# Performance work log

Hardware: AMD Instinct MI355X
Metric: run time of the kernel (lower is better)

## Reference

```python
import jax, jax.numpy as jnp
import numpy as np

# --- dims (match init_kwargs) ---
VOCAB = 16; D_MODEL = 512; NLAYERS = 4; LMAX = 1024; NCLASSES = 2
D_STATE = 128; D_CONV = 4; EXPAND = 2; HEADDIM = 64; PAD_IDX = 4
D_INNER = EXPAND * D_MODEL            # 1024
NHEADS = D_INNER // HEADDIM           # 16
CONV_DIM = D_INNER + 2 * D_STATE      # 1280 (ngroups=1)
D_IN_PROJ = 2 * D_INNER + 2 * D_STATE + NHEADS  # 2320
BATCH = 8; SEQ = 1024
EPS = 1e-5


def silu(x):
    return x * jax.nn.sigmoid(x)


def setup_inputs() -> dict:
    key = jax.random.key(0)
    ks = jax.random.split(key, 24)
    s = 0.02
    emb = jax.random.normal(ks[0], (VOCAB, D_MODEL), jnp.float32) * s
    emb = emb.at[PAD_IDX].set(0.0)  # padding_idx row is zero
    inp = {
        "tokens": jax.random.randint(ks[1], (BATCH, SEQ), 0, VOCAB),
        "attention_mask": jnp.ones((BATCH, SEQ), jnp.float32),
        "emb": emb,
        "pos_emb": jax.random.normal(ks[2], (1, LMAX, D_MODEL), jnp.float32) * s,
        "inp_w": jax.random.normal(ks[3], (D_MODEL, D_MODEL), jnp.float32) * s,
        "inp_b": jnp.zeros((D_MODEL,), jnp.float32),
        "ln_g": jnp.ones((D_MODEL,), jnp.float32),
        "ln_b": jnp.zeros((D_MODEL,), jnp.float32),
        # stacked per-layer Mamba2 params
        "in_proj_w": jax.random.normal(ks[4], (NLAYERS, D_IN_PROJ, D_MODEL), jnp.float32) * s,
        "conv_w": jax.random.normal(ks[5], (NLAYERS, CONV_DIM, D_CONV), jnp.float32) * 0.2,
        "conv_b": jnp.zeros((NLAYERS, CONV_DIM), jnp.float32),
        "dt_bias": jax.random.uniform(ks[6], (NLAYERS, NHEADS), jnp.float32, -4.0, -1.0),
        "A_log": jnp.log(jax.random.uniform(ks[7], (NLAYERS, NHEADS), jnp.float32, 1.0, 16.0)),
        "Dparam": jnp.ones((NLAYERS, NHEADS), jnp.float32),
        "norm_w": jnp.ones((NLAYERS, D_INNER), jnp.float32),
        "out_proj_w": jax.random.normal(ks[8], (NLAYERS, D_MODEL, D_INNER), jnp.float32) * s,
        "pooler_w": jax.random.normal(ks[9], (D_MODEL, D_MODEL), jnp.float32) * s,
        "pooler_b": jnp.zeros((D_MODEL,), jnp.float32),
        "cls_w1": jax.random.normal(ks[10], (D_MODEL // 2, D_MODEL), jnp.float32) * s,
        "cls_b1": jnp.zeros((D_MODEL // 2,), jnp.float32),
        "cls_w2": jax.random.normal(ks[11], (NCLASSES, D_MODEL // 2), jnp.float32) * s,
        "cls_b2": jnp.zeros((NCLASSES,), jnp.float32),
    }
    return inp


def mamba2_block(x, in_proj_w, conv_w, conv_b, dt_bias, A_log, Dp, norm_w, out_proj_w):
    """Mamba2 (ngroups=1, no proj biases, conv bias) on x:(B,L,d_model)."""
    Bsz, L, _ = x.shape
    zxbcdt = jnp.einsum("bld,ed->ble", x, in_proj_w)  # (B,L,2320)
    z = zxbcdt[..., :D_INNER]
    xBC = zxbcdt[..., D_INNER:D_INNER + CONV_DIM]
    dt = zxbcdt[..., D_INNER + CONV_DIM:]             # (B,L,H)
    # causal depthwise conv1d + silu
    xp = jnp.pad(xBC, ((0, 0), (D_CONV - 1, 0), (0, 0)))
    conv = conv_b
    for k in range(D_CONV):
        conv = conv + xp[:, k:k + L, :] * conv_w[:, k]
    xBC = silu(conv)
    xh = xBC[..., :D_INNER].reshape(Bsz, L, NHEADS, HEADDIM)
    Bc = xBC[..., D_INNER:D_INNER + D_STATE]          # (B,L,N)
    Cc = xBC[..., D_INNER + D_STATE:]                 # (B,L,N)
    dt = jax.nn.softplus(dt + dt_bias)                # (B,L,H)
    A = -jnp.exp(A_log)                               # (H,)
    dA = jnp.exp(dt * A)                              # (B,L,H)

    def step(h, inp):
        x_t, B_t, C_t, dt_t, dA_t = inp  # (B,H,P),(B,N),(B,N),(B,H),(B,H)
        h = h * dA_t[:, :, None, None] + (dt_t[:, :, None] * x_t)[..., None] * B_t[:, None, None, :]
        y = jnp.einsum("bhpn,bn->bhp", h, C_t)
        return h, y

    h0 = jnp.zeros((Bsz, NHEADS, HEADDIM, D_STATE), x.dtype)
    xs = (xh.transpose(1, 0, 2, 3), Bc.transpose(1, 0, 2), Cc.transpose(1, 0, 2),
          dt.transpose(1, 0, 2), dA.transpose(1, 0, 2))
    _, ys = jax.lax.scan(step, h0, xs)                # (L,B,H,P)
    y = ys.transpose(1, 0, 2, 3) + Dp[None, None, :, None] * xh
    y = y.reshape(Bsz, L, D_INNER)
    # gated RMSNorm: rmsnorm(y * silu(z)) * weight
    y = y * silu(z)
    y = y * jax.lax.rsqrt(jnp.mean(y * y, axis=-1, keepdims=True) + EPS) * norm_w
    return jnp.einsum("ble,de->bld", y, out_proj_w)


def reference(tokens, attention_mask, emb, pos_emb, inp_w, inp_b, ln_g, ln_b,
              in_proj_w, conv_w, conv_b, dt_bias, A_log, Dparam, norm_w, out_proj_w,
              pooler_w, pooler_b, cls_w1, cls_b1, cls_w2, cls_b2):
    L = tokens.shape[1]
    x = emb[tokens] + pos_emb[:, :L, :]
    # input_block: Linear -> LayerNorm (dropout is identity at eval)
    x = jnp.einsum("bld,ed->ble", x, inp_w) + inp_b
    mu = jnp.mean(x, -1, keepdims=True)
    var = jnp.mean((x - mu) ** 2, -1, keepdims=True)
    x = (x - mu) * jax.lax.rsqrt(var + EPS) * ln_g + ln_b
    x = x * attention_mask[..., None]
    for i in range(NLAYERS):
        res = x
        x = mamba2_block(x, in_proj_w[i], conv_w[i], conv_b[i], dt_bias[i],
                         A_log[i], Dparam[i], norm_w[i], out_proj_w[i])
        x = res + x
        x = x * attention_mask[..., None]
    pooled = (jnp.mean(x, axis=1) + jnp.max(x, axis=1)) * 0.5
    pooled = jax.nn.gelu(jnp.einsum("bd,ed->be", pooled, pooler_w) + pooler_b)
    h = jax.nn.gelu(jnp.einsum("bd,ed->be", pooled, cls_w1) + cls_b1)
    return jnp.einsum("bd,ed->be", h, cls_w2) + cls_b2
```

## Files before the change

### kernel.cpp

```cpp
#include <hip/hip_runtime.h>

#define EPS 1e-5f
typedef unsigned short u16;
typedef short s16x8 __attribute__((ext_vector_type(8)));
typedef float f32x4 __attribute__((ext_vector_type(4)));

__device__ __forceinline__ float siluf(float x) { return x / (1.0f + __expf(-x)); }
__device__ __forceinline__ float geluf(float x) {
    float u = 0.7978845608028654f * (x + 0.044715f * x * x * x);
    return 0.5f * x * (1.0f + tanhf(u));
}
__device__ __forceinline__ u16 f2bf(float f) {
    unsigned u = __float_as_uint(f);
    return (u16)((u + 0x7fffu + ((u >> 16) & 1u)) >> 16);
}
__device__ __forceinline__ float bf2f(u16 v) {
    return __uint_as_float(((unsigned)v) << 16);
}
struct u16x4 { u16 x, y, z, w; };
__device__ __forceinline__ u16x4 f2bf4(float4 v) {
    u16x4 r; r.x = f2bf(v.x); r.y = f2bf(v.y); r.z = f2bf(v.z); r.w = f2bf(v.w);
    return r;
}

#define GLOAD_LDS16(gp, lp) __builtin_amdgcn_global_load_lds( \
    (const __attribute__((address_space(1))) void*)(gp),      \
    (__attribute__((address_space(3))) void*)(lp), 16, 0, 0)

__global__ void k_casts(const float* __restrict__ ip, const float* __restrict__ op,
                        const float* __restrict__ inp, u16* __restrict__ wip,
                        u16* __restrict__ wop, u16* __restrict__ winp,
                        const int* __restrict__ tok, const float* __restrict__ emb,
                        const float* __restrict__ pos, u16* __restrict__ xe) {
    int idx = blockIdx.x * 256 + threadIdx.x;
    if (idx < 1245184) {
        int e4 = idx * 4;
        int layer = e4 / 1245184;
        int rem   = e4 - layer * 1245184;
        int row   = rem >> 9;
        int k     = rem & 511;
        float4 v = make_float4(0.f, 0.f, 0.f, 0.f);
        if (row < 2320)
            v = *(const float4*)(ip + (size_t)layer * 1187840 + (size_t)row * 512 + k);
        *(u16x4*)(wip + e4) = f2bf4(v);
    } else if (idx < 1245184 + 524288) {
        int j = idx - 1245184;
        float4 v = *(const float4*)(op + (size_t)j * 4);
        *(u16x4*)(wop + (size_t)j * 4) = f2bf4(v);
    } else if (idx < 1245184 + 524288 + 65536) {
        int j = idx - 1245184 - 524288;
        float4 v = *(const float4*)(inp + (size_t)j * 4);
        *(u16x4*)(winp + (size_t)j * 4) = f2bf4(v);
    } else if (idx < 1835008 + 1048576) {
        int j = idx - 1835008;
        int d4 = j & 127;
        int bl = j >> 7;
        int l  = bl & 1023;
        float4 e = *(const float4*)(emb + tok[bl] * 512 + d4 * 4);
        float4 p = *(const float4*)(pos + l * 512 + d4 * 4);
        float4 v = make_float4(e.x + p.x, e.y + p.y, e.z + p.z, e.w + p.w);
        *(u16x4*)(xe + (size_t)j * 4) = f2bf4(v);
    }
}

#define STAGE_I(buf, k0) do {                                                   \
    _Pragma("unroll")                                                           \
    for (int s_ = 0; s_ < 2; s_++) {                                            \
        int g_ = w * 2 + s_;                                                    \
        GLOAD_LDS16(A + (size_t)(m0 + g_ * 16 + lr) * 512 + (k0) + lk,          \
                    smem + (buf) * 8192 + g_ * 512);                            \
    }                                                                           \
    GLOAD_LDS16(B + (size_t)(n0 + w * 16 + lr) * 512 + (k0) + lk,               \
                smem + 24576 + (buf) * 4096 + w * 512);                         \
    } while (0)

#define COMPUTE_I(buf) do {                                                     \
    s16x8 af_[4], bf_[4];                                                       \
    _Pragma("unroll")                                                           \
    for (int i_ = 0; i_ < 4; i_++) {                                            \
        af_[i_] = *(const s16x8*)&smem[(buf) * 8192 + (wr * 4 + i_) * 512 + l * 8]; \
        bf_[i_] = *(const s16x8*)&smem[24576 + (buf) * 4096 + (wc * 4 + i_) * 512 + l * 8]; \
    }                                                                           \
    _Pragma("unroll")                                                           \
    for (int i_ = 0; i_ < 4; i_++)                                              \
        _Pragma("unroll")                                                       \
        for (int j_ = 0; j_ < 4; j_++)                                          \
            acc[i_][j_] = __builtin_amdgcn_mfma_f32_16x16x32_bf16(              \
                af_[i_], bf_[j_], acc[i_][j_], 0, 0, 0);                        \
    } while (0)

__global__ __launch_bounds__(512, 4) void k_gemm_in(
    const u16* __restrict__ A, const u16* __restrict__ B,
    u16* __restrict__ zbf, u16* __restrict__ xbcbf, float* __restrict__ dtw) {
    __shared__ __align__(16) u16 smem[36864];
    const int t = threadIdx.x;
    const int w = t >> 6, l = t & 63;
    const int wr = w >> 1, wc = w & 1;
    const int lr = l & 15, lk = (l >> 4) * 8;
    const int wgid = (blockIdx.x & 7) * 76 + (blockIdx.x >> 3);
    const int m0 = (wgid / 19) * 256;
    const int nt = wgid % 19;
    const int n0 = nt * 128;

    f32x4 acc[4][4] = {};

    STAGE_I(0, 0);
    STAGE_I(1, 32);
    for (int ki = 0; ki < 14; ki++) {
        asm volatile("s_waitcnt vmcnt(3)" ::: "memory");
        __builtin_amdgcn_s_barrier();
        STAGE_I((ki + 2) % 3, (ki + 2) * 32);
        COMPUTE_I(ki % 3);
    }
    asm volatile("s_waitcnt vmcnt(3)" ::: "memory");
    __builtin_amdgcn_s_barrier();
    COMPUTE_I(14 % 3);
    asm volatile("s_waitcnt vmcnt(0)" ::: "memory");
    __builtin_amdgcn_s_barrier();
    COMPUTE_I(15 % 3);
    __syncthreads();

    if (nt < 18) {
#pragma unroll
        for (int i = 0; i < 4; i++)
#pragma unroll
            for (int j = 0; j < 4; j++)
#pragma unroll
                for (int r2 = 0; r2 < 4; r2++) {
                    int erow = wr * 64 + i * 16 + (l >> 4) * 4 + r2;
                    int ecol = wc * 64 + j * 16 + (l & 15);
                    smem[erow * 136 + ecol] = f2bf(acc[i][j][r2]);
                }
        __syncthreads();
        if (nt < 8) {
#pragma unroll
            for (int it = 0; it < 8; it++) {
                int v = it * 512 + t;
                int row = v >> 4, col = (v & 15) * 8;
                *(s16x8*)&zbf[(size_t)(m0 + row) * 1024 + n0 + col] =
                    *(const s16x8*)&smem[row * 136 + col];
            }
        } else {
            int nb = n0 - 1024;
#pragma unroll
            for (int it = 0; it < 8; it++) {
                int v = it * 512 + t;
                int row = v >> 4, col = (v & 15) * 8;
                *(s16x8*)&xbcbf[(size_t)(m0 + row) * 1280 + nb + col] =
                    *(const s16x8*)&smem[row * 136 + col];
            }
        }
    } else {
#pragma unroll
        for (int i = 0; i < 4; i++) {
            int mb = m0 + wr * 64 + i * 16 + (l >> 4) * 4;
#pragma unroll
            for (int j = 0; j < 4; j++) {
                int n = n0 + wc * 64 + j * 16 + (l & 15);
#pragma unroll
                for (int r2 = 0; r2 < 4; r2++) {
                    if (n < 2320)
                        dtw[(size_t)(mb + r2) * 16 + (n - 2304)] = acc[i][j][r2];
                }
            }
        }
    }
}

#define STAGE(buf, k0) do {                                                     \
    GLOAD_LDS16(A + (size_t)(m0 + w * 16 + lr) * K + (k0) + lk,                 \
                &Asm[buf][w * 512]);                                            \
    GLOAD_LDS16(B + (size_t)(n0 + w * 16 + lr) * K + (k0) + lk,                 \
                &Bsm[buf][w * 512]);                                            \
    } while (0)

#define COMPUTE(buf) do {                                                       \
    s16x8 af_[4], bf_[2];                                                       \
    _Pragma("unroll")                                                           \
    for (int i_ = 0; i_ < 4; i_++)                                              \
        af_[i_] = *(const s16x8*)&Asm[buf][(wr * 4 + i_) * 512 + l * 8];        \
    _Pragma("unroll")                                                           \
    for (int j_ = 0; j_ < 2; j_++)                                              \
        bf_[j_] = *(const s16x8*)&Bsm[buf][(wc * 2 + j_) * 512 + l * 8];        \
    _Pragma("unroll")                                                           \
    for (int i_ = 0; i_ < 4; i_++)                                              \
        _Pragma("unroll")                                                       \
        for (int j_ = 0; j_ < 2; j_++)                                          \
            acc[i_][j_] = __builtin_amdgcn_mfma_f32_16x16x32_bf16(              \
                af_[i_], bf_[j_], acc[i_][j_], 0, 0, 0);                        \
    } while (0)

template <int MODE>
__global__ __launch_bounds__(512) void k_gemm_mfma(
    const u16* __restrict__ A, const u16* __restrict__ B,
    const float* __restrict__ bias, float* __restrict__ C,
    u16* __restrict__ Cbf, const float* __restrict__ mask,
    int M, int N, int K, int gx) {
    __shared__ u16 Asm[3][4096];
    __shared__ u16 Bsm[3][4096];
    const int t = threadIdx.x;
    const int w = t >> 6, l = t & 63;
    const int wr = w >> 2, wc = w & 3;
    const int lr = l & 15, lk = (l >> 4) * 8;
    const int nwg = gridDim.x;
    const int q = nwg >> 3, r = nwg & 7;
    const int x8 = blockIdx.x & 7, d8 = blockIdx.x >> 3;
    const int wgid = (x8 < r) ? x8 * (q + 1) + d8 : r * (q + 1) + (x8 - r) * q + d8;
    const int m0 = (wgid / gx) * 128;
    const int n0 = (wgid % gx) * 128;

    f32x4 acc[4][2] = {};

    const int nk = K >> 5;
    STAGE(0, 0);
    STAGE(1, 32);
    for (int ki = 0; ki < nk - 2; ki++) {
        asm volatile("s_waitcnt vmcnt(2)" ::: "memory");
        __builtin_amdgcn_s_barrier();
        STAGE((ki + 2) % 3, (ki + 2) * 32);
        COMPUTE(ki % 3);
    }
    asm volatile("s_waitcnt vmcnt(2)" ::: "memory");
    __builtin_amdgcn_s_barrier();
    COMPUTE((nk - 2) % 3);
    asm volatile("s_waitcnt vmcnt(0)" ::: "memory");
    __builtin_amdgcn_s_barrier();
    COMPUTE((nk - 1) % 3);

#pragma unroll
    for (int i = 0; i < 4; i++) {
        int mb = m0 + wr * 64 + i * 16 + (l >> 4) * 4;
#pragma unroll
        for (int j = 0; j < 2; j++) {
            int n = n0 + wc * 32 + j * 16 + (l & 15);
#pragma unroll
            for (int r2 = 0; r2 < 4; r2++) {
                int m = mb + r2;
                float v = acc[i][j][r2];
                if (n < N) {
                    size_t o = (size_t)m * N + n;
                    if (MODE == 1) {
                        C[o] = v + bias[n];
                    } else {
                        float v2 = (bf2f(Cbf[o]) + v) * mask[m];
                        Cbf[o] = f2bf(v2);
                    }
                }
            }
        }
    }
}

__global__ __launch_bounds__(128) void k_layernorm(
    const float* __restrict__ x, const float* __restrict__ g,
    const float* __restrict__ b, const float* __restrict__ mask,
    u16* __restrict__ xbf) {
    __shared__ float2 sbuf[2];
    int bl = blockIdx.x;
    int t  = threadIdx.x;
    float4 v = *(const float4*)(x + (size_t)bl * 512 + t * 4);
    float s = v.x + v.y + v.z + v.w;
    float q = v.x * v.x + v.y * v.y + v.z * v.z + v.w * v.w;
    for (int off = 32; off; off >>= 1) {
        s += __shfl_xor(s, off, 64);
        q += __shfl_xor(q, off, 64);
    }
    int wid = t >> 6, lane = t & 63;
    if (lane == 0) sbuf[wid] = make_float2(s, q);
    __syncthreads();
    float ts = sbuf[0].x + sbuf[1].x;
    float tq = sbuf[0].y + sbuf[1].y;
    float mu  = ts * (1.f / 512.f);
    float var = tq * (1.f / 512.f) - mu * mu;
    float inv = 1.0f / sqrtf(var + EPS);
    float mk  = mask[bl];
    float4 gg = *(const float4*)(g + t * 4);
    float4 bb = *(const float4*)(b + t * 4);
    float4 o;
    o.x = ((v.x - mu) * inv * gg.x + bb.x) * mk;
    o.y = ((v.y - mu) * inv * gg.y + bb.y) * mk;
    o.z = ((v.z - mu) * inv * gg.z + bb.z) * mk;
    o.w = ((v.w - mu) * inv * gg.w + bb.w) * mk;
    *(u16x4*)(xbf + (size_t)bl * 512 + t * 4) = f2bf4(o);
}

__global__ __launch_bounds__(320) void k_conv(
    const u16* __restrict__ xbc_in, const float* __restrict__ cw,
    const float* __restrict__ cb, u16* __restrict__ xhbf,
    u16* __restrict__ bcbf) {
    int bid = blockIdx.x;
    int bl = (bid & 7) * 1024 + (bid >> 3);
    int l  = bl & 1023;
    int c  = threadIdx.x * 4;
    float4 w0 = *(const float4*)(cw + (c + 0) * 4);
    float4 w1 = *(const float4*)(cw + (c + 1) * 4);
    float4 w2 = *(const float4*)(cw + (c + 2) * 4);
    float4 w3 = *(const float4*)(cw + (c + 3) * 4);
    float4 a  = *(const float4*)(cb + c);
#pragma unroll
    for (int k = 0; k < 4; k++) {
        if (l + k - 3 >= 0) {
            u16x4 v = *(const u16x4*)(xbc_in + (size_t)(bl + k - 3) * 1280 + c);
            const float* wk0 = (const float*)&w0;
            const float* wk1 = (const float*)&w1;
            const float* wk2 = (const float*)&w2;
            const float* wk3 = (const float*)&w3;
            a.x = fmaf(bf2f(v.x), wk0[k], a.x);
            a.y = fmaf(bf2f(v.y), wk1[k], a.y);
            a.z = fmaf(bf2f(v.z), wk2[k], a.z);
            a.w = fmaf(bf2f(v.w), wk3[k], a.w);
        }
    }
    float4 o = make_float4(siluf(a.x), siluf(a.y), siluf(a.z), siluf(a.w));
    if (c < 1024)
        *(u16x4*)(xhbf + (size_t)bl * 1024 + c) = f2bf4(o);
    else
        *(u16x4*)(bcbf + (size_t)bl * 256 + (c - 1024)) = f2bf4(o);
}

#define SSD_STAGE(dst, k0) do {                                                 \
    _Pragma("unroll")                                                           \
    for (int s_ = 0; s_ < 2; s_++) {                                            \
        int g_ = w * 2 + s_;                                                    \
        GLOAD_LDS16(bcbf + (row0 + g_ * 16 + lr) * 256 + 128 + (k0) + lk8,      \
                    (dst) + g_ * 512);                                          \
        GLOAD_LDS16(bcbf + (row0 + g_ * 16 + lr) * 256 + (k0) + lk8,            \
                    (dst) + 4096 + g_ * 512);                                   \
    } } while (0)

__global__ __launch_bounds__(256) void k_ssd(
    const u16* __restrict__ xhbf, const u16* __restrict__ bcbf,
    const float* __restrict__ dt_raw, const float* __restrict__ dtbias,
    const float* __restrict__ alog, float* __restrict__ elbuf,
    u16* __restrict__ y16, u16* __restrict__ scb16) {
    int bid = blockIdx.x;
    int bhc = (bid & 7) * 128 + (bid >> 3);
    int c = bhc & 7, h = (bhc >> 3) & 15, b = bhc >> 7;
    const size_t row0 = (size_t)b * 1024 + c * 128;
    const int t = threadIdx.x, w = t >> 6, l = t & 63;
    const int wr = w >> 1, wc = w & 1;
    const int lr = l & 15, lk8 = (l >> 4) * 8;

    __shared__ float cl[128], dtl[128], wv[128];
    __shared__ float csh;
    __shared__ __align__(16) u16 shA[8704];
    __shared__ __align__(16) u16 shB[17408];

    float dtb_h = dtbias[h];
    float A = -__expf(alog[h]);
    float raw = 0.f;
    if (t < 128) raw = dt_raw[(row0 + t) * 16 + h] + dtb_h;
    SSD_STAGE(shA, 0);
    SSD_STAGE(shB, 32);

    float v = 0.f;
    if (t < 128) {
        float s = (raw > 20.f) ? raw : log1pf(__expf(raw));
        dtl[t] = s;
        v = s * A;
        int lane = t & 63;
#pragma unroll
        for (int off = 1; off < 64; off <<= 1) {
            float o = __shfl_up(v, off, 64);
            if (lane >= off) v += o;
        }
        if (t == 63) csh = v;
    }
    __syncthreads();
    if (t >= 64 && t < 128) v += csh;
    if (t < 128) {
        cl[t] = v;
        elbuf[(size_t)bhc * 128 + t] = __expf(v);
    }
    __syncthreads();
    if (t < 128) wv[t] = __expf(cl[127] - cl[t]);

    f32x4 acc[4][4] = {};
    for (int ks = 0; ks < 4; ks++) {
        u16* cur = (ks & 1) ? shB : shA;
        if (ks < 3) asm volatile("s_waitcnt vmcnt(4)" ::: "memory");
        else        asm volatile("s_waitcnt vmcnt(0)" ::: "memory");
        __builtin_amdgcn_s_barrier();
        s16x8 af[4], bfr[4];
#pragma unroll
        for (int i = 0; i < 4; i++) {
            af[i]  = *(const s16x8*)&cur[(wr * 4 + i) * 512 + l * 8];
            bfr[i] = *(const s16x8*)&cur[4096 + (wc * 4 + i) * 512 + l * 8];
        }
#pragma unroll
        for (int i = 0; i < 4; i++)
#pragma unroll
            for (int j = 0; j < 4; j++)
                acc[i][j] = __builtin_amdgcn_mfma_f32_16x16x32_bf16(af[i], bfr[j], acc[i][j], 0, 0, 0);
        __builtin_amdgcn_s_barrier();
        if (ks + 2 < 4) SSD_STAGE(cur, (ks + 2) * 32);
    }

    {
        int j = t >> 1;
        int ph = (t & 1) * 32;
        float dj = dtl[j];
        const u16* src = xhbf + (row0 + j) * 1024 + h * 64 + ph;
#pragma unroll
        for (int vq = 0; vq < 4; vq++) {
            s16x8 vec = *(const s16x8*)(src + vq * 8);
            int p0 = ph + vq * 8;
#pragma unroll
            for (int i = 0; i < 8; i++)
                shA[(p0 + i) * 136 + j] = f2bf(dj * bf2f((u16)vec[i]));
        }
    }
    __syncthreads();

    f32x4 acc2[4][2] = {};
    for (int half = 0; half < 2; half++) {
        if (wc == half) {
#pragma unroll
            for (int i = 0; i < 4; i++) {
#pragma unroll
                for (int j = 0; j < 4; j++) {
                    int col = half * 64 + j * 16 + (l & 15);
#pragma unroll
                    for (int r = 0; r < 4; r++) {
                        int row = wr * 64 + i * 16 + (l >> 4) * 4 + r;
                        float e = __expf(fminf(cl[row] - cl[col], 0.f));
                        float pv = (col <= row) ? acc[i][j][r] * e : 0.f;
                        shB[row * 72 + j * 16 + (l & 15)] = f2bf(pv);
                    }
                }
            }
        }
        __syncthreads();
#pragma unroll
        for (int ks = 0; ks < 2; ks++) {
            int kof = ks * 32;
            s16x8 pa[4], ub[2];
#pragma unroll
            for (int i = 0; i < 4; i++)
                pa[i] = *(const s16x8*)&shB[(wr * 64 + i * 16 + lr) * 72 + kof + lk8];
#pragma unroll
            for (int jj = 0; jj < 2; jj++)
                ub[jj] = *(const s16x8*)&shA[(wc * 32 + jj * 16 + lr) * 136 + half * 64 + kof + lk8];
#pragma unroll
            for (int i = 0; i < 4; i++)
#pragma unroll
                for (int jj = 0; jj < 2; jj++)
                    acc2[i][jj] = __builtin_amdgcn_mfma_f32_16x16x32_bf16(pa[i], ub[jj], acc2[i][jj], 0, 0, 0);
        }
        __syncthreads();
    }

    {
        float* fb = (float*)shB;
#pragma unroll
        for (int i = 0; i < 4; i++)
#pragma unroll
            for (int jj = 0; jj < 2; jj++)
#pragma unroll
                for (int r = 0; r < 4; r++) {
                    int row = wr * 64 + i * 16 + (l >> 4) * 4 + r;
                    fb[row * 68 + wc * 32 + jj * 16 + (l & 15)] = acc2[i][jj][r];
                }
        __syncthreads();
#pragma unroll
        for (int it = 0; it < 4; it++) {
            int vv = it * 256 + t;
            int row = vv >> 3, col = (vv & 7) * 8;
            float4 f0 = *(const float4*)&fb[row * 68 + col];
            float4 f1 = *(const float4*)&fb[row * 68 + col + 4];
            s16x8 ov;
            const float* p0 = (const float*)&f0;
            const float* p1 = (const float*)&f1;
#pragma unroll
            for (int j = 0; j < 4; j++) { ov[j] = (short)f2bf(p0[j]); ov[4 + j] = (short)f2bf(p1[j]); }
            *(s16x8*)&y16[(row0 + row) * 1024 + h * 64 + col] = ov;
        }
        __syncthreads();
    }

    {
        int j = t >> 1;
        int nh = (t & 1) * 64;
        float wj = wv[j];
        const u16* src = bcbf + (row0 + j) * 256 + nh;
#pragma unroll
        for (int vq = 0; vq < 8; vq++) {
            s16x8 vec = *(const s16x8*)(src + vq * 8);
            int n0 = nh + vq * 8;
#pragma unroll
            for (int i = 0; i < 8; i++)
                shB[(n0 + i) * 136 + j] = f2bf(wj * bf2f((u16)vec[i]));
        }
    }
    __syncthreads();

    f32x4 acc3[4][2] = {};
#pragma unroll
    for (int ks = 0; ks < 4; ks++) {
        int kof = ks * 32;
        s16x8 ua[4], bb[2];
#pragma unroll
        for (int i = 0; i < 4; i++)
            ua[i] = *(const s16x8*)&shA[(i * 16 + lr) * 136 + kof + lk8];
#pragma unroll
        for (int jj = 0; jj < 2; jj++)
            bb[jj] = *(const s16x8*)&shB[(w * 32 + jj * 16 + lr) * 136 + kof + lk8];
#pragma unroll
        for (int i = 0; i < 4; i++)
#pragma unroll
            for (int jj = 0; jj < 2; jj++)
                acc3[i][jj] = __builtin_amdgcn_mfma_f32_16x16x32_bf16(ua[i], bb[jj], acc3[i][jj], 0, 0, 0);
    }
#pragma unroll
    for (int i = 0; i < 4; i++)
#pragma unroll
        for (int jj = 0; jj < 2; jj++) {
            int n = w * 32 + jj * 16 + (l & 15);
#pragma unroll
            for (int r = 0; r < 4; r++) {
                int p = i * 16 + (l >> 4) * 4 + r;
                scb16[(size_t)bhc * 8192 + (size_t)p * 128 + n] = f2bf(acc3[i][jj][r]);
            }
        }
}

__global__ __launch_bounds__(256) void k_states(u16* __restrict__ scb16,
                                                const float* __restrict__ elbuf) {
    int bh  = blockIdx.x >> 1;
    int seg = blockIdx.x & 1;
    int t = threadIdx.x;
    float hreg[16];
#pragma unroll
    for (int j = 0; j < 16; j++) hreg[j] = 0.f;
    size_t o = (size_t)(seg * 256 + t) * 16;
    for (int c = 0; c < 8; c++) {
        int bhc = bh * 8 + c;
        float Tc = elbuf[(size_t)bhc * 128 + 127];
        u16* p = scb16 + (size_t)bhc * 8192 + o;
        s16x8 v0 = *(s16x8*)(p);
        s16x8 v1 = *(s16x8*)(p + 8);
        s16x8 o0, o1;
#pragma unroll
        for (int j = 0; j < 8; j++) {
            o0[j] = (short)f2bf(hreg[j]);
            o1[j] = (short)f2bf(hreg[8 + j]);
        }
        *(s16x8*)(p)     = o0;
        *(s16x8*)(p + 8) = o1;
#pragma unroll
        for (int j = 0; j < 8; j++) {
            hreg[j]     = fmaf(Tc, hreg[j],     bf2f((u16)v0[j]));
            hreg[8 + j] = fmaf(Tc, hreg[8 + j], bf2f((u16)v1[j]));
        }
    }
}

#define INT_STAGE(bf_, k0_) do {                                                \
    _Pragma("unroll")                                                           \
    for (int s_ = 0; s_ < 2; s_++) {                                            \
        int g_ = w * 2 + s_;                                                    \
        GLOAD_LDS16(bcbf + (row0 + g_ * 16 + lr) * 256 + 128 + (k0_) + lk8,     \
                    &CStg[bf_][g_ * 512]);                                      \
    }                                                                           \
    GLOAD_LDS16(scb16 + (size_t)bhc * 8192 + (size_t)(w * 16 + lr) * 128 + (k0_) + lk8, \
                &HStg[bf_][w * 512]);                                           \
    } while (0)

__global__ __launch_bounds__(256) void k_inter(
    const u16* __restrict__ xhbf, const u16* __restrict__ bcbf,
    const float* __restrict__ elbuf, const u16* __restrict__ scb16,
    const float* __restrict__ Dp, u16* __restrict__ y16) {
    int bid = blockIdx.x;
    int bhc = (bid & 7) * 128 + (bid >> 3);
    int c = bhc & 7, h = (bhc >> 3) & 15, b = bhc >> 7;
    const size_t row0 = (size_t)b * 1024 + c * 128;
    const int t = threadIdx.x, w = t >> 6, l = t & 63;
    const int wr = w >> 1, wc = w & 1;
    const int lr = l & 15, lk8 = (l >> 4) * 8;
    __shared__ __align__(16) u16 CStg[2][4096];
    __shared__ __align__(16) u16 HStg[2][2048];
    __shared__ __align__(16) float FY[64 * 68];
    __shared__ float el[128];
    float Dv = Dp[h];
    float elv = (t < 128) ? elbuf[(size_t)bhc * 128 + t] : 0.f;

    INT_STAGE(0, 0);
    INT_STAGE(1, 32);
    if (t < 128) el[t] = elv;

    f32x4 acc[4][2] = {};
    for (int ks = 0; ks < 4; ks++) {
        int cur = ks & 1;
        if (ks < 3) asm volatile("s_waitcnt vmcnt(3)" ::: "memory");
        else        asm volatile("s_waitcnt vmcnt(0)" ::: "memory");
        __builtin_amdgcn_s_barrier();
        s16x8 ca[4], hb[2];
#pragma unroll
        for (int i = 0; i < 4; i++)
            ca[i] = *(const s16x8*)&CStg[cur][(wr * 4 + i) * 512 + l * 8];
#pragma unroll
        for (int jj = 0; jj < 2; jj++)
            hb[jj] = *(const s16x8*)&HStg[cur][(wc * 2 + jj) * 512 + l * 8];
#pragma unroll
        for (int i = 0; i < 4; i++)
#pragma unroll
            for (int jj = 0; jj < 2; jj++)
                acc[i][jj] = __builtin_amdgcn_mfma_f32_16x16x32_bf16(ca[i], hb[jj], acc[i][jj], 0, 0, 0);
        __builtin_amdgcn_s_barrier();
        if (ks + 2 < 4) INT_STAGE(cur, (ks + 2) * 32);
    }

    for (int ch = 0; ch < 2; ch++) {
        if (wr == ch) {
#pragma unroll
            for (int i = 0; i < 4; i++)
#pragma unroll
                for (int jj = 0; jj < 2; jj++)
#pragma unroll
                    for (int r = 0; r < 4; r++) {
                        int rrow = i * 16 + (l >> 4) * 4 + r;
                        FY[rrow * 68 + wc * 32 + jj * 16 + (l & 15)] =
                            el[ch * 64 + rrow] * acc[i][jj][r];
                    }
        }
        __syncthreads();
#pragma unroll
        for (int it = 0; it < 2; it++) {
            int vv = it * 256 + t;
            int row = vv >> 3, col = (vv & 7) * 8;
            float4 f0 = *(const float4*)&FY[row * 68 + col];
            float4 f1 = *(const float4*)&FY[row * 68 + col + 4];
            size_t yo = (row0 + ch * 64 + row) * 1024 + h * 64 + col;
            s16x8 yv = *(const s16x8*)&y16[yo];
            s16x8 xv = *(const s16x8*)&xhbf[yo];
            s16x8 ov;
            const float* p0 = (const float*)&f0;
            const float* p1 = (const float*)&f1;
#pragma unroll
            for (int j = 0; j < 4; j++) {
                ov[j]     = (short)f2bf(bf2f((u16)yv[j])     + p0[j] + Dv * bf2f((u16)xv[j]));
                ov[4 + j] = (short)f2bf(bf2f((u16)yv[4 + j]) + p1[j] + Dv * bf2f((u16)xv[4 + j]));
            }
            *(s16x8*)&y16[yo] = ov;
        }
        __syncthreads();
    }
}

__global__ __launch_bounds__(256) void k_gate(
    const u16* __restrict__ y16, const u16* __restrict__ zbf,
    const float* __restrict__ nw, u16* __restrict__ ybf) {
    __shared__ float sbuf[4];
    int bl = blockIdx.x;
    int t  = threadIdx.x;
    u16x4 yv4 = *(const u16x4*)(y16 + (size_t)bl * 1024 + t * 4);
    u16x4 zv4 = *(const u16x4*)(zbf + (size_t)bl * 1024 + t * 4);
    float4 gv;
    gv.x = bf2f(yv4.x) * siluf(bf2f(zv4.x));
    gv.y = bf2f(yv4.y) * siluf(bf2f(zv4.y));
    gv.z = bf2f(yv4.z) * siluf(bf2f(zv4.z));
    gv.w = bf2f(yv4.w) * siluf(bf2f(zv4.w));
    float q = gv.x * gv.x + gv.y * gv.y + gv.z * gv.z + gv.w * gv.w;
    for (int off = 32; off; off >>= 1) q += __shfl_xor(q, off, 64);
    int wid = t >> 6, lane = t & 63;
    if (lane == 0) sbuf[wid] = q;
    __syncthreads();
    float tot = sbuf[0] + sbuf[1] + sbuf[2] + sbuf[3];
    float scale = 1.0f / sqrtf(tot * (1.f / 1024.f) + EPS);
    float4 nv = *(const float4*)(nw + t * 4);
    float4 o;
    o.x = gv.x * scale * nv.x;
    o.y = gv.y * scale * nv.y;
    o.z = gv.z * scale * nv.z;
    o.w = gv.w * scale * nv.w;
    *(u16x4*)(ybf + (size_t)bl * 1024 + t * 4) = f2bf4(o);
}

__global__ __launch_bounds__(256) void k_pool1(const u16* __restrict__ xbf,
                                               float* __restrict__ psum,
                                               float* __restrict__ pmax) {
    int blk = blockIdx.x;
    int b = blk >> 6, lc = blk & 63;
    int t = threadIdx.x;
    const u16* px = xbf + (size_t)b * 524288 + (size_t)lc * 16 * 512;
    float s0 = 0.f, s1 = 0.f, m0 = -3.0e38f, m1 = -3.0e38f;
#pragma unroll
    for (int r = 0; r < 16; r++) {
        float v0 = bf2f(px[r * 512 + t]);
        float v1 = bf2f(px[r * 512 + t + 256]);
        s0 += v0; s1 += v1;
        m0 = fmaxf(m0, v0); m1 = fmaxf(m1, v1);
    }
    psum[(size_t)blk * 512 + t]       = s0;
    psum[(size_t)blk * 512 + t + 256] = s1;
    pmax[(size_t)blk * 512 + t]       = m0;
    pmax[(size_t)blk * 512 + t + 256] = m1;
}

__global__ __launch_bounds__(256) void k_pool2(const float* __restrict__ psum,
                                               const float* __restrict__ pmax,
                                               float* __restrict__ pooled) {
    int idx = blockIdx.x * 256 + threadIdx.x;
    int b = idx >> 9, d = idx & 511;
    float s = 0.f, m = -3.0e38f;
    for (int c = 0; c < 64; c++) {
        s += psum[((size_t)b * 64 + c) * 512 + d];
        m = fmaxf(m, pmax[((size_t)b * 64 + c) * 512 + d]);
    }
    pooled[idx] = 0.5f * (s * (1.f / 1024.f) + m);
}

template <int ACT>
__global__ void k_fc(const float* __restrict__ in, const float* __restrict__ W,
                     const float* __restrict__ bias, float* __restrict__ out,
                     int BN, int N, int K) {
    int idx = blockIdx.x * 64 + threadIdx.x;
    if (idx >= BN) return;
    int b = idx / N, n = idx % N;
    const float* a = in + (size_t)b * K;
    const float* w = W + (size_t)n * K;
    float acc = 0.f;
    for (int k = 0; k < K; k += 4) {
        float4 av = *(const float4*)(a + k);
        float4 wv = *(const float4*)(w + k);
        acc += av.x * wv.x + av.y * wv.y + av.z * wv.z + av.w * wv.w;
    }
    float v = acc + bias[n];
    if (ACT == 1) v = geluf(v);
    out[idx] = v;
}

extern "C" void kernel_launch(void* const* d_in, const int* in_sizes, int n_in,
                              void* d_out, int out_size, void* d_ws, size_t ws_size,
                              hipStream_t stream) {
    (void)in_sizes; (void)n_in; (void)out_size; (void)ws_size;
    const int*   tok        = (const int*)  d_in[0];
    const float* mask       = (const float*)d_in[1];
    const float* emb        = (const float*)d_in[2];
    const float* pos        = (const float*)d_in[3];
    const float* inp_w      = (const float*)d_in[4];
    const float* inp_b      = (const float*)d_in[5];
    const float* ln_g       = (const float*)d_in[6];
    const float* ln_b       = (const float*)d_in[7];
    const float* in_proj_w  = (const float*)d_in[8];
    const float* conv_w     = (const float*)d_in[9];
    const float* conv_b     = (const float*)d_in[10];
    const float* dt_bias    = (const float*)d_in[11];
    const float* A_log      = (const float*)d_in[12];
    const float* Dparam     = (const float*)d_in[13];
    const float* norm_w     = (const float*)d_in[14];
    const float* out_proj_w = (const float*)d_in[15];
    const float* pooler_w   = (const float*)d_in[16];
    const float* pooler_b   = (const float*)d_in[17];
    const float* cls_w1     = (const float*)d_in[18];
    const float* cls_b1     = (const float*)d_in[19];
    const float* cls_w2     = (const float*)d_in[20];
    const float* cls_b2     = (const float*)d_in[21];
    float* out = (float*)d_out;

    float* ws     = (float*)d_ws;
    float* x      = ws;
    float* dt_raw = x + (size_t)8192 * 512;
    float* elbuf  = dt_raw + (size_t)8192 * 16;
    float* psum   = elbuf + 131072;
    float* pmax   = psum + 262144;
    float* pooled = pmax + 262144;
    float* pbuf   = pooled + 4096;
    float* cbuf   = pbuf + 4096;
    u16* x_bf    = (u16*)(cbuf + 2048);
    u16* z_bf    = x_bf + (size_t)8192 * 512;
    u16* xbc_in  = z_bf + (size_t)8192 * 1024;
    u16* y_bf    = xbc_in + (size_t)8192 * 1280;
    u16* xhbf    = y_bf + (size_t)8192 * 1024;
    u16* bcbf    = xhbf + (size_t)8192 * 1024;
    u16* y16     = bcbf + (size_t)8192 * 256;
    u16* wip_bf  = y16 + (size_t)8192 * 1024;
    u16* wop_bf  = wip_bf + (size_t)4 * 2432 * 512;
    u16* winp_bf = wop_bf + (size_t)4 * 512 * 1024;
    u16* xe_bf   = (u16*)y16;
    u16* scb16   = xbc_in;

    k_casts<<<11264, 256, 0, stream>>>(in_proj_w, out_proj_w, inp_w,
                                       wip_bf, wop_bf, winp_bf,
                                       tok, emb, pos, xe_bf);

    k_gemm_mfma<1><<<256, 512, 0, stream>>>(xe_bf, winp_bf, inp_b, x, nullptr,
                                            nullptr, 8192, 512, 512, 4);
    k_layernorm<<<8192, 128, 0, stream>>>(x, ln_g, ln_b, mask, x_bf);

    for (int i = 0; i < 4; i++) {
        k_gemm_in<<<608, 512, 0, stream>>>(x_bf, wip_bf + (size_t)i * 2432 * 512,
                                           z_bf, xbc_in, dt_raw);
        k_conv<<<8192, 320, 0, stream>>>(xbc_in, conv_w + (size_t)i * 1280 * 4,
                                         conv_b + (size_t)i * 1280, xhbf, bcbf);
        k_ssd<<<1024, 256, 0, stream>>>(xhbf, bcbf, dt_raw, dt_bias + i * 16,
                                        A_log + i * 16, elbuf, y16, scb16);
        k_states<<<256, 256, 0, stream>>>(scb16, elbuf);
        k_inter<<<1024, 256, 0, stream>>>(xhbf, bcbf, elbuf, scb16,
                                          Dparam + (size_t)i * 16, y16);
        k_gate<<<8192, 256, 0, stream>>>(y16, z_bf, norm_w + (size_t)i * 1024, y_bf);
        k_gemm_mfma<2><<<256, 512, 0, stream>>>(y_bf, wop_bf + (size_t)i * 512 * 1024,
                                                nullptr, nullptr, x_bf, mask,
                                                8192, 512, 1024, 4);
    }

    k_pool1<<<512, 256, 0, stream>>>(x_bf, psum, pmax);
    k_pool2<<<16, 256, 0, stream>>>(psum, pmax, pooled);
    k_fc<1><<<64, 64, 0, stream>>>(pooled, pooler_w, pooler_b, pbuf, 8 * 512, 512, 512);
    k_fc<1><<<32, 64, 0, stream>>>(pbuf, cls_w1, cls_b1, cbuf, 8 * 256, 256, 512);
    k_fc<0><<<1, 64, 0, stream>>>(cbuf, cls_w2, cls_b2, out, 8 * 2, 2, 256);
}
```

Before: 808.8 us.

## Fuse inter-chunk state scan into k_inter, drop k_states kernel

Removes the separate sequential k_states kernel that turned per-chunk states into prefix states in place. Each k_inter block now rebuilds its own incoming state by summing the earlier chunks' states, weighted by cumulative decay products, and writes the result into a full-size LDS buffer before the MFMA loop. This saves one launch and a read-modify-write pass over the state buffer per layer. In exchange, later chunks do redundant O(c) global reads, LDS use grows, and there is an extra bf16 rounding difference.

```diff
diff --git a/kernel.cpp b/kernel.cpp
--- a/kernel.cpp
+++ b/kernel.cpp
@@ -524,47 +524,13 @@
         }
 }
 
-__global__ __launch_bounds__(256) void k_states(u16* __restrict__ scb16,
-                                                const float* __restrict__ elbuf) {
-    int bh  = blockIdx.x >> 1;
-    int seg = blockIdx.x & 1;
-    int t = threadIdx.x;
-    float hreg[16];
-#pragma unroll
-    for (int j = 0; j < 16; j++) hreg[j] = 0.f;
-    size_t o = (size_t)(seg * 256 + t) * 16;
-    for (int c = 0; c < 8; c++) {
-        int bhc = bh * 8 + c;
-        float Tc = elbuf[(size_t)bhc * 128 + 127];
-        u16* p = scb16 + (size_t)bhc * 8192 + o;
-        s16x8 v0 = *(s16x8*)(p);
-        s16x8 v1 = *(s16x8*)(p + 8);
-        s16x8 o0, o1;
-#pragma unroll
-        for (int j = 0; j < 8; j++) {
-            o0[j] = (short)f2bf(hreg[j]);
-            o1[j] = (short)f2bf(hreg[8 + j]);
-        }
-        *(s16x8*)(p)     = o0;
-        *(s16x8*)(p + 8) = o1;
-#pragma unroll
-        for (int j = 0; j < 8; j++) {
-            hreg[j]     = fmaf(Tc, hreg[j],     bf2f((u16)v0[j]));
-            hreg[8 + j] = fmaf(Tc, hreg[8 + j], bf2f((u16)v1[j]));
-        }
-    }
-}
-
 #define INT_STAGE(bf_, k0_) do {                                                \
     _Pragma("unroll")                                                           \
     for (int s_ = 0; s_ < 2; s_++) {                                            \
         int g_ = w * 2 + s_;                                                    \
         GLOAD_LDS16(bcbf + (row0 + g_ * 16 + lr) * 256 + 128 + (k0_) + lk8,     \
                     &CStg[bf_][g_ * 512]);                                      \
-    }                                                                           \
-    GLOAD_LDS16(scb16 + (size_t)bhc * 8192 + (size_t)(w * 16 + lr) * 128 + (k0_) + lk8, \
-                &HStg[bf_][w * 512]);                                           \
-    } while (0)
+    } } while (0)
 
 __global__ __launch_bounds__(256) void k_inter(
     const u16* __restrict__ xhbf, const u16* __restrict__ bcbf,
@@ -573,12 +539,13 @@
     int bid = blockIdx.x;
     int bhc = (bid & 7) * 128 + (bid >> 3);
     int c = bhc & 7, h = (bhc >> 3) & 15, b = bhc >> 7;
+    int bh = bhc >> 3;
     const size_t row0 = (size_t)b * 1024 + c * 128;
     const int t = threadIdx.x, w = t >> 6, l = t & 63;
     const int wr = w >> 1, wc = w & 1;
     const int lr = l & 15, lk8 = (l >> 4) * 8;
     __shared__ __align__(16) u16 CStg[2][4096];
-    __shared__ __align__(16) u16 HStg[2][2048];
+    __shared__ __align__(16) u16 Hsm[8192];
     __shared__ __align__(16) float FY[64 * 68];
     __shared__ float el[128];
     float Dv = Dp[h];
@@ -588,10 +555,35 @@
     INT_STAGE(1, 32);
     if (t < 128) el[t] = elv;
 
+    {
+        int hrow = w * 16 + lr;
+        const u16* base = scb16 + (size_t)bh * 8 * 8192 + (size_t)hrow * 128;
+#pragma unroll
+        for (int ks = 0; ks < 4; ks++) {
+            const u16* src0 = base + ks * 32 + lk8;
+            float f8[8];
+#pragma unroll
+            for (int i = 0; i < 8; i++) f8[i] = 0.f;
+            float p = 1.f;
+            for (int j = c - 1; j >= 0; j--) {
+                s16x8 v = *(const s16x8*)(src0 + (size_t)j * 8192);
+#pragma unroll
+                for (int i = 0; i < 8; i++)
+                    f8[i] = fmaf(p, bf2f((u16)v[i]), f8[i]);
+                p *= elbuf[((size_t)(bh * 8 + j)) * 128 + 127];
+            }
+            s16x8 o;
+#pragma unroll
+            for (int i = 0; i < 8; i++) o[i] = (short)f2bf(f8[i]);
+            *(s16x8*)&Hsm[ks * 2048 + w * 512 + l * 8] = o;
+        }
+    }
+    __syncthreads();
+
     f32x4 acc[4][2] = {};
     for (int ks = 0; ks < 4; ks++) {
         int cur = ks & 1;
-        if (ks < 3) asm volatile("s_waitcnt vmcnt(3)" ::: "memory");
+        if (ks < 3) asm volatile("s_waitcnt vmcnt(2)" ::: "memory");
         else        asm volatile("s_waitcnt vmcnt(0)" ::: "memory");
         __builtin_amdgcn_s_barrier();
         s16x8 ca[4], hb[2];
@@ -600,7 +592,7 @@
             ca[i] = *(const s16x8*)&CStg[cur][(wr * 4 + i) * 512 + l * 8];
 #pragma unroll
         for (int jj = 0; jj < 2; jj++)
-            hb[jj] = *(const s16x8*)&HStg[cur][(wc * 2 + jj) * 512 + l * 8];
+            hb[jj] = *(const s16x8*)&Hsm[ks * 2048 + (wc * 2 + jj) * 512 + l * 8];
 #pragma unroll
         for (int i = 0; i < 4; i++)
 #pragma unroll
@@ -795,7 +787,6 @@
                                          conv_b + (size_t)i * 1280, xhbf, bcbf);
         k_ssd<<<1024, 256, 0, stream>>>(xhbf, bcbf, dt_raw, dt_bias + i * 16,
                                         A_log + i * 16, elbuf, y16, scb16);
-        k_states<<<256, 256, 0, stream>>>(scb16, elbuf);
         k_inter<<<1024, 256, 0, stream>>>(xhbf, bcbf, elbuf, scb16,
                                           Dparam + (size_t)i * 16, y16);
         k_gate<<<8192, 256, 0, stream>>>(y16, z_bf, norm_w + (size_t)i * 1024, y_bf);
```

Result: no change. 821.8 us (+1.6%).
